# Optimization experiments

Hardware: AMD Instinct MI355X
Metric: run time of the kernel (lower is better)

## Reference

```python
import jax, jax.numpy as jnp
import numpy as np

NUM_HEADS = 8


def setup_inputs() -> dict:
    key = jax.random.key(0)
    ks = jax.random.split(key, 6)
    B, C, H, W = 64, 512, 16, 16
    x = jax.random.normal(ks[0], (B, C, H, W), dtype=jnp.float32)
    qkv_w = jax.random.normal(ks[1], (3 * C, C), dtype=jnp.float32) * (C ** -0.5)
    qkv_b = jax.random.normal(ks[2], (3 * C,), dtype=jnp.float32) * 0.02
    out_w = jax.random.normal(ks[3], (C, C), dtype=jnp.float32) * (C ** -0.5)
    out_b = jax.random.normal(ks[4], (C,), dtype=jnp.float32) * 0.02
    rel_pos_enc = jax.random.normal(ks[5], (NUM_HEADS, 2 * 16 - 1, 2 * 16 - 1), dtype=jnp.float32) * 0.02
    return {"x": x, "qkv_w": qkv_w, "qkv_b": qkv_b, "out_w": out_w,
            "out_b": out_b, "rel_pos_enc": rel_pos_enc}


def _attention(x, qkv_w, qkv_b, out_w, out_b, rel_pos_enc):
    B, C, H, W = x.shape
    heads = rel_pos_enc.shape[0]
    hd = C // heads
    N = H * W

    # 1x1 conv qkv projection == pointwise GEMM over channels
    qkv = jnp.einsum('bchw,oc->bohw', x, qkv_w) + qkv_b[None, :, None, None]
    q, k, v = jnp.split(qkv, 3, axis=1)  # each (B, C, H, W)
    q = q.reshape(B, heads, hd, N)
    k = k.reshape(B, heads, hd, N)
    v = v.reshape(B, heads, hd, N)

    attn = jnp.einsum('bhdn,bhdm->bhnm', q, k) * (hd ** -0.5)  # (B,h,N,N)

    # gathered 2D relative position bias: bias[head,(h1,w1),(h2,w2)] =
    #   rel_pos_enc[head, h1-h2+15, w1-w2+15]
    h_idx = (jnp.arange(H)[:, None] - jnp.arange(H)[None, :]) + 16 - 1  # (H,H)
    w_idx = (jnp.arange(W)[:, None] - jnp.arange(W)[None, :]) + 16 - 1  # (W,W)
    bias = rel_pos_enc[:, h_idx[:, None, :, None], w_idx[None, :, None, :]]  # (h,H,W,H,W)
    bias = bias.reshape(heads, N, N)

    attn = jax.nn.softmax(attn + bias[None], axis=-1)
    out = jnp.einsum('bhnm,bhdm->bhdn', attn, v).reshape(B, C, H, W)
    out = jnp.einsum('bchw,oc->bohw', out, out_w) + out_b[None, :, None, None]
    return out


def reference(x, qkv_w, qkv_b, out_w, out_b, rel_pos_enc):
    return _attention(x, qkv_w, qkv_b, out_w, out_b, rel_pos_enc)
```

## Files before the change

### kernel.cpp

```cpp
#include <hip/hip_runtime.h>

typedef __attribute__((ext_vector_type(8))) short short8;
typedef __attribute__((ext_vector_type(4))) float floatx4;
typedef __attribute__((ext_vector_type(4))) int   intx4;

#define MFMA16(a,b,c) __builtin_amdgcn_mfma_f32_16x16x32_bf16((a),(b),(c),0,0,0)

static __device__ __forceinline__ unsigned short f2bf(float f){
    unsigned int u = __float_as_uint(f);
    u = (u + 0x7FFFu + ((u >> 16) & 1u)) >> 16;
    return (unsigned short)u;
}

static __device__ __forceinline__ unsigned int pkbf(float lo, float hi){
    unsigned int r;
    asm("v_cvt_pk_bf16_f32 %0, %1, %2" : "=v"(r) : "v"(lo), "v"(hi));
    return r;
}

static __device__ __forceinline__ void async16(const unsigned short* g, const unsigned short* l){
    __builtin_amdgcn_global_load_lds(
        (const __attribute__((address_space(1))) unsigned int*)g,
        (__attribute__((address_space(3))) unsigned int*)l, 16, 0, 0);
}

__global__ __launch_bounds__(256) void k_prep(const float* __restrict__ x,
                                              unsigned short* __restrict__ xT,
                                              const float* __restrict__ qkvw,
                                              unsigned short* __restrict__ wqkv,
                                              const float* __restrict__ outw,
                                              unsigned short* __restrict__ wout,
                                              const float* __restrict__ rel,
                                              unsigned short* __restrict__ Bp){
    __shared__ unsigned short tile[64][78];
    const int bid = blockIdx.x;
    const int tid = threadIdx.x;
    if (bid < 2048){
        const int c0 = (bid & 7) * 64;
        const int n0 = ((bid >> 3) & 3) * 64;
        const int b  = bid >> 5;
        const int chunk = tid & 7;
        const int r     = tid >> 3;
        const float*    src = x  + (size_t)b * 131072;
        unsigned short* dst = xT + (size_t)b * 131072;
#pragma unroll
        for (int it = 0; it < 2; ++it){
            int c = r + it * 32;
            const float* p = src + (size_t)(c0 + c) * 256 + n0 + chunk * 8;
            float4 f0 = *(const float4*)(p);
            float4 f1 = *(const float4*)(p + 4);
            short8 v;
            v[0]=(short)f2bf(f0.x); v[1]=(short)f2bf(f0.y); v[2]=(short)f2bf(f0.z); v[3]=(short)f2bf(f0.w);
            v[4]=(short)f2bf(f1.x); v[5]=(short)f2bf(f1.y); v[6]=(short)f2bf(f1.z); v[7]=(short)f2bf(f1.w);
            *(short8*)&tile[c][chunk * 8] = v;
        }
        __syncthreads();
#pragma unroll
        for (int it = 0; it < 2; ++it){
            int n = r + it * 32;
            short8 o;
#pragma unroll
            for (int e = 0; e < 8; ++e) o[e] = (short)tile[chunk * 8 + e][n];
            *(short8*)(dst + (size_t)(n0 + n) * 512 + c0 + chunk * 8) = o;
        }
    } else if (bid < 3072){
        int i = (bid - 2048) * 256 + tid;
        const float* s; unsigned short* d; int j;
        if (i < 196608){ s = qkvw; d = wqkv; j = i; }
        else { j = i - 196608; if (j >= 65536) return; s = outw; d = wout; }
        float4 f = *(const float4*)(s + (size_t)j * 4);
        uint2 v;
        v.x = (unsigned int)f2bf(f.x) | ((unsigned int)f2bf(f.y) << 16);
        v.y = (unsigned int)f2bf(f.z) | ((unsigned int)f2bf(f.w) << 16);
        *(uint2*)(d + (size_t)j * 4) = v;
    } else {
        int idx  = (bid - 3072) * 256 + tid;
        int lane = idx & 63;
        int ct   = (idx >> 6) & 15;
        int pp   = (idx >> 10) & 1;
        int wv   = (idx >> 11) & 7;
        int h    = idx >> 14;
        int token = wv * 32 + pp * 16 + (lane & 15);
        int key0  = 32 * (ct >> 1) + 8 * (lane >> 4) + 4 * (ct & 1);
        int th = token >> 4, tw = token & 15;
        int kh = key0 >> 4,  kw0 = key0 & 15;
        int base = h * 961 + (th - kh + 15) * 31 + (tw - kw0 + 15);
        float v0 = rel[base]     * 1.44269504f;
        float v1 = rel[base - 1] * 1.44269504f;
        float v2 = rel[base - 2] * 1.44269504f;
        float v3 = rel[base - 3] * 1.44269504f;
        uint2 o; o.x = pkbf(v0, v1); o.y = pkbf(v2, v3);
        *(uint2*)(Bp + (size_t)idx * 4) = o;
    }
}

__global__ __launch_bounds__(512, 2) void k_fused(const unsigned short* __restrict__ xT,
                                                  const unsigned short* __restrict__ wbf,
                                                  const float* __restrict__ qkvb,
                                                  const unsigned short* __restrict__ Bp,
                                                  unsigned short* __restrict__ ao){
    __shared__ unsigned short SH[77824];
    const int XS = 0;
    const int WS = 16384;
    const int QS = 28672;
    const int KS = 45056;
    const int VS = 61440;

    const int bid  = blockIdx.x;
    const int xcd  = bid & 7;
    const int slot = bid >> 3;
    const int b = xcd * 8 + (slot & 7);
    const int h = slot >> 3;
    const int tid  = threadIdx.x;
    const int wave = tid >> 6;
    const int lane = tid & 63;
    const int lrow = lane & 15;
    const int lgrp = lane >> 4;
    const int mq = wave >> 1;
    const int nh = wave & 1;

    floatx4 acc[4][6];
#pragma unroll
    for (int i = 0; i < 4; ++i)
#pragma unroll
        for (int j = 0; j < 6; ++j){ floatx4 z = {0.f,0.f,0.f,0.f}; acc[i][j] = z; }

    const unsigned short* xb = xT + (size_t)(b * 256) * 512;
    const unsigned short* xsrc[4]; int xdo[4];
#pragma unroll
    for (int c = 0; c < 4; ++c){
        int s   = (c * 8 + wave) * 64 + lane;
        int row = s >> 3, pch = s & 7;
        int sch = pch ^ (row & 7);
        xsrc[c] = xb + (size_t)row * 512 + sch * 8;
        xdo[c]  = (c * 8 + wave) * 512;
    }
    const unsigned short* wsrc[3]; int wdo[3];
#pragma unroll
    for (int c = 0; c < 3; ++c){
        int s   = (c * 8 + wave) * 64 + lane;
        int row = s >> 3, pch = s & 7;
        int sch = pch ^ (row & 7);
        int grow = (row >> 6) * 512 + h * 64 + (row & 63);
        wsrc[c] = wbf + (size_t)grow * 512 + sch * 8;
        wdo[c]  = (c * 8 + wave) * 512;
    }

    auto stageA = [&](int XBs, int WBs, int kk){
#pragma unroll
        for (int c = 0; c < 4; ++c) async16(xsrc[c] + kk, &SH[XBs + xdo[c]]);
#pragma unroll
        for (int c = 0; c < 3; ++c) async16(wsrc[c] + kk, &SH[WBs + wdo[c]]);
    };
    auto compA = [&](int XBs, int WBs){
#pragma unroll
        for (int ks = 0; ks < 2; ++ks){
            short8 af[4], bq[6];
#pragma unroll
            for (int mt = 0; mt < 4; ++mt){
                int row = mq * 64 + mt * 16 + lrow;
                int pch = (ks * 4 + lgrp) ^ (row & 7);
                af[mt] = *(const short8*)&SH[XBs + row * 64 + pch * 8];
            }
#pragma unroll
            for (int nt = 0; nt < 6; ++nt){
                int row = nh * 96 + nt * 16 + lrow;
                int pch = (ks * 4 + lgrp) ^ (row & 7);
                bq[nt] = *(const short8*)&SH[WBs + row * 64 + pch * 8];
            }
#pragma unroll
            for (int mt = 0; mt < 4; ++mt)
#pragma unroll
                for (int nt = 0; nt < 6; ++nt)
                    acc[mt][nt] = MFMA16(af[mt], bq[nt], acc[mt][nt]);
        }
    };

    stageA(XS, WS, 0);
    stageA(QS, KS, 64);
#pragma unroll
    for (int t2 = 0; t2 < 4; ++t2){
        asm volatile("s_waitcnt vmcnt(7)" ::: "memory");
        __builtin_amdgcn_s_barrier();
        asm volatile("" ::: "memory");
        compA(XS, WS);
        asm volatile("" ::: "memory");
        if (t2 < 3){
            __builtin_amdgcn_s_barrier();
            stageA(XS, WS, t2 * 128 + 128);
            asm volatile("s_waitcnt vmcnt(7)" ::: "memory");
        } else {
            asm volatile("s_waitcnt vmcnt(0)" ::: "memory");
        }
        __builtin_amdgcn_s_barrier();
        asm volatile("" ::: "memory");
        compA(QS, KS);
        asm volatile("" ::: "memory");
        __builtin_amdgcn_s_barrier();
        if (t2 < 3) stageA(QS, KS, t2 * 128 + 192);
    }

    const uint2* bpw = (const uint2*)Bp + (((size_t)h * 8 + wave) * 2) * 1024 + lane;
    uint2 bA[16], bB[16];
#pragma unroll
    for (int ct = 0; ct < 16; ++ct){
        bA[ct] = bpw[ct * 64];
        bB[ct] = bpw[(16 + ct) * 64];
    }
    asm volatile("" ::: "memory");

#pragma unroll
    for (int mt = 0; mt < 4; ++mt){
#pragma unroll
        for (int nt = 0; nt < 6; ++nt){
            int col = nh * 96 + nt * 16 + lrow;
            int seg = col >> 6, off = col & 63;
            float bv = qkvb[seg * 512 + h * 64 + off];
            int token0 = mq * 64 + mt * 16 + lgrp * 4;
            if (seg == 2){
                int lch = token0 >> 3;
                int pch = (lch & 24) | ((lch & 7) ^ (off & 7));
                uint2 vv;
                vv.x = pkbf(acc[mt][nt][0] + bv, acc[mt][nt][1] + bv);
                vv.y = pkbf(acc[mt][nt][2] + bv, acc[mt][nt][3] + bv);
                *(uint2*)&SH[VS + off * 256 + pch * 8 + (lgrp & 1) * 4] = vv;
            } else if (seg == 1){
#pragma unroll
                for (int r = 0; r < 4; ++r){
                    int token = token0 + r;
                    int kslot = (token & ~0x1C) | ((token & 4) << 2) | ((token & 0x18) >> 1);
                    int pch   = (off >> 3) ^ (kslot & 7);
                    SH[KS + kslot * 64 + pch * 8 + (off & 7)] = f2bf(acc[mt][nt][r] + bv);
                }
            } else {
#pragma unroll
                for (int r = 0; r < 4; ++r){
                    int token = token0 + r;
                    int pch   = (off >> 3) ^ (token & 7);
                    SH[QS + token * 64 + pch * 8 + (off & 7)] =
                        f2bf((acc[mt][nt][r] + bv) * 0.18033688f);
                }
            }
        }
    }
    __syncthreads();

    short8 aq[2][2];
#pragma unroll
    for (int pp = 0; pp < 2; ++pp)
#pragma unroll
        for (int kc = 0; kc < 2; ++kc){
            int row = wave * 32 + pp * 16 + lrow;
            int pch = (kc * 4 + lgrp) ^ (row & 7);
            aq[pp][kc] = *(const short8*)&SH[QS + row * 64 + pch * 8];
        }

    floatx4 st0[16], st1[16];
    __builtin_amdgcn_s_setprio(1);
#pragma unroll
    for (int ct = 0; ct < 16; ++ct){
        int row  = ct * 16 + lrow;
        int pch0 = lgrp ^ (row & 7);
        short8 k0 = *(const short8*)&SH[KS + row * 64 + pch0 * 8];
        short8 k1 = *(const short8*)&SH[KS + row * 64 + (pch0 ^ 4) * 8];
        floatx4 z0, z1;
        z0[0] = __uint_as_float(bA[ct].x << 16);
        z0[1] = __uint_as_float(bA[ct].x & 0xFFFF0000u);
        z0[2] = __uint_as_float(bA[ct].y << 16);
        z0[3] = __uint_as_float(bA[ct].y & 0xFFFF0000u);
        z1[0] = __uint_as_float(bB[ct].x << 16);
        z1[1] = __uint_as_float(bB[ct].x & 0xFFFF0000u);
        z1[2] = __uint_as_float(bB[ct].y << 16);
        z1[3] = __uint_as_float(bB[ct].y & 0xFFFF0000u);
        z0 = MFMA16(k0, aq[0][0], z0);
        z0 = MFMA16(k1, aq[0][1], z0);
        z1 = MFMA16(k0, aq[1][0], z1);
        z1 = MFMA16(k1, aq[1][1], z1);
        st0[ct] = z0; st1[ct] = z1;
    }
    __builtin_amdgcn_s_setprio(0);

    float inv0, inv1;
    {
        float p0=0.f,p1=0.f,p2=0.f,p3=0.f;
#pragma unroll
        for (int ct = 0; ct < 16; ++ct){
            float e0 = __builtin_amdgcn_exp2f(st0[ct][0]); st0[ct][0]=e0; p0+=e0;
            float e1 = __builtin_amdgcn_exp2f(st0[ct][1]); st0[ct][1]=e1; p1+=e1;
            float e2 = __builtin_amdgcn_exp2f(st0[ct][2]); st0[ct][2]=e2; p2+=e2;
            float e3 = __builtin_amdgcn_exp2f(st0[ct][3]); st0[ct][3]=e3; p3+=e3;
        }
        float s = (p0+p1)+(p2+p3);
        s += __shfl_xor(s, 16, 64);
        s += __shfl_xor(s, 32, 64);
        inv0 = 1.f / s;
    }
    {
        float p0=0.f,p1=0.f,p2=0.f,p3=0.f;
#pragma unroll
        for (int ct = 0; ct < 16; ++ct){
            float e0 = __builtin_amdgcn_exp2f(st1[ct][0]); st1[ct][0]=e0; p0+=e0;
            float e1 = __builtin_amdgcn_exp2f(st1[ct][1]); st1[ct][1]=e1; p1+=e1;
            float e2 = __builtin_amdgcn_exp2f(st1[ct][2]); st1[ct][2]=e2; p2+=e2;
            float e3 = __builtin_amdgcn_exp2f(st1[ct][3]); st1[ct][3]=e3; p3+=e3;
        }
        float s = (p0+p1)+(p2+p3);
        s += __shfl_xor(s, 16, 64);
        s += __shfl_xor(s, 32, 64);
        inv1 = 1.f / s;
    }

    intx4 pf0[8], pf1[8];
#pragma unroll
    for (int ms = 0; ms < 8; ++ms){
        intx4 t0_, t1_;
        t0_.x = (int)pkbf(st0[2*ms  ][0], st0[2*ms  ][1]);
        t0_.y = (int)pkbf(st0[2*ms  ][2], st0[2*ms  ][3]);
        t0_.z = (int)pkbf(st0[2*ms+1][0], st0[2*ms+1][1]);
        t0_.w = (int)pkbf(st0[2*ms+1][2], st0[2*ms+1][3]);
        pf0[ms] = t0_;
        t1_.x = (int)pkbf(st1[2*ms  ][0], st1[2*ms  ][1]);
        t1_.y = (int)pkbf(st1[2*ms  ][2], st1[2*ms  ][3]);
        t1_.z = (int)pkbf(st1[2*ms+1][0], st1[2*ms+1][1]);
        t1_.w = (int)pkbf(st1[2*ms+1][2], st1[2*ms+1][3]);
        pf1[ms] = t1_;
    }

    unsigned short* aob = ao + (size_t)(b * 256) * 512 + h * 64;
    const int n0 = wave * 32 + lrow;
    __builtin_amdgcn_s_setprio(1);
#pragma unroll
    for (int dt = 0; dt < 4; ++dt){
        floatx4 a0 = {0.f,0.f,0.f,0.f}, a1 = {0.f,0.f,0.f,0.f};
#pragma unroll
        for (int ms = 0; ms < 8; ++ms){
            int row = dt * 16 + lrow;
            int lch = ms * 4 + lgrp;
            int pch = (lch & 24) | ((lch & 7) ^ (row & 7));
            short8 vb = *(const short8*)&SH[VS + row * 256 + pch * 8];
            a0 = MFMA16(vb, __builtin_bit_cast(short8, pf0[ms]), a0);
            a1 = MFMA16(vb, __builtin_bit_cast(short8, pf1[ms]), a1);
        }
        uint2 o0, o1;
        o0.x = pkbf(a0[0] * inv0, a0[1] * inv0);
        o0.y = pkbf(a0[2] * inv0, a0[3] * inv0);
        *(uint2*)(aob + (size_t)n0 * 512 + dt * 16 + lgrp * 4) = o0;
        o1.x = pkbf(a1[0] * inv1, a1[1] * inv1);
        o1.y = pkbf(a1[2] * inv1, a1[3] * inv1);
        *(uint2*)(aob + (size_t)(n0 + 16) * 512 + dt * 16 + lgrp * 4) = o1;
    }
    __builtin_amdgcn_s_setprio(0);
}

__global__ __launch_bounds__(256, 2) void k_out(const unsigned short* __restrict__ ao,
                                                const unsigned short* __restrict__ wbf,
                                                const float* __restrict__ bias,
                                                float* __restrict__ out){
    __shared__ unsigned short Ash[2][2][128][32];
    __shared__ unsigned short Bsh[2][2][128][32];
    const int bid  = blockIdx.x;
    const int xcd  = bid & 7;
    const int slot = bid >> 3;
    const int t0 = (xcd * 16 + (slot & 15)) * 128;
    const int o0 = (slot >> 4) * 128;
    const int tid  = threadIdx.x;
    const int wave = tid >> 6;
    const int lane = tid & 63;
    const int lrow = lane & 15;
    const int wm   = (wave >> 1) * 64;
    const int wn   = (wave & 1) * 64;
    const int ld_row = wave * 32 + (lane >> 2);
    const int ld_col = (((lane & 3) ^ ((lane >> 3) & 3))) * 8;
    const int pcho = (((lane >> 4) ^ ((lrow >> 1) & 3))) * 8;

    floatx4 acc[4][4];
#pragma unroll
    for (int i = 0; i < 4; ++i)
#pragma unroll
        for (int j = 0; j < 4; ++j){ floatx4 z = {0.f,0.f,0.f,0.f}; acc[i][j] = z; }

    const unsigned short* gA = wbf + (size_t)(o0 + ld_row) * 512 + ld_col;
    const unsigned short* gB = ao  + (size_t)(t0 + ld_row) * 512 + ld_col;

    auto stage = [&](int d, int kk){
        async16(gA + kk,                 &Ash[d][0][wave * 32][0]);
        async16(gA + kk + 16 * 512,      &Ash[d][0][wave * 32 + 16][0]);
        async16(gA + kk + 32,            &Ash[d][1][wave * 32][0]);
        async16(gA + kk + 32 + 16 * 512, &Ash[d][1][wave * 32 + 16][0]);
        async16(gB + kk,                 &Bsh[d][0][wave * 32][0]);
        async16(gB + kk + 16 * 512,      &Bsh[d][0][wave * 32 + 16][0]);
        async16(gB + kk + 32,            &Bsh[d][1][wave * 32][0]);
        async16(gB + kk + 32 + 16 * 512, &Bsh[d][1][wave * 32 + 16][0]);
    };
    auto comp = [&](int d){
#pragma unroll
        for (int s = 0; s < 2; ++s){
            short8 af[4], bq[4];
#pragma unroll
            for (int mt = 0; mt < 4; ++mt) af[mt] = *(const short8*)&Ash[d][s][wm + mt*16 + lrow][pcho];
#pragma unroll
            for (int nt = 0; nt < 4; ++nt) bq[nt] = *(const short8*)&Bsh[d][s][wn + nt*16 + lrow][pcho];
#pragma unroll
            for (int mt = 0; mt < 4; ++mt)
#pragma unroll
                for (int nt = 0; nt < 4; ++nt)
                    acc[mt][nt] = MFMA16(af[mt], bq[nt], acc[mt][nt]);
        }
    };

    stage(0, 0);
    stage(1, 64);
#pragma unroll
    for (int t2 = 0; t2 < 4; ++t2){
        asm volatile("s_waitcnt vmcnt(8)" ::: "memory");
        __builtin_amdgcn_s_barrier();
        asm volatile("" ::: "memory");
        comp(0);
        asm volatile("" ::: "memory");
        if (t2 < 3){
            __builtin_amdgcn_s_barrier();
            stage(0, t2 * 128 + 128);
            asm volatile("s_waitcnt vmcnt(8)" ::: "memory");
        } else {
            asm volatile("s_waitcnt vmcnt(0)" ::: "memory");
        }
        __builtin_amdgcn_s_barrier();
        asm volatile("" ::: "memory");
        comp(1);
        asm volatile("" ::: "memory");
        __builtin_amdgcn_s_barrier();
        if (t2 < 3) stage(1, t2 * 128 + 192);
    }
#pragma unroll
    for (int mt = 0; mt < 4; ++mt){
        int orow0 = o0 + wm + mt*16 + (lane >> 4) * 4;
#pragma unroll
        for (int nt = 0; nt < 4; ++nt){
            int tcol = t0 + wn + nt*16 + lrow;
            int bb = tcol >> 8, nn = tcol & 255;
#pragma unroll
            for (int r = 0; r < 4; ++r){
                float bv = bias[orow0 + r];
                out[(size_t)(bb * 512 + orow0 + r) * 256 + nn] = acc[mt][nt][r] + bv;
            }
        }
    }
}

extern "C" void kernel_launch(void* const* d_in, const int* in_sizes, int n_in,
                              void* d_out, int out_size, void* d_ws, size_t ws_size,
                              hipStream_t stream){
    const float* x    = (const float*)d_in[0];
    const float* qkvw = (const float*)d_in[1];
    const float* qkvb = (const float*)d_in[2];
    const float* outw = (const float*)d_in[3];
    const float* outb = (const float*)d_in[4];
    const float* rel  = (const float*)d_in[5];
    float* out = (float*)d_out;

    const size_t XT_OFF = 0;
    const size_t AO_OFF = 16777216;
    const size_t W_OFF  = 33554432;
    const size_t NEED   = W_OFF + 4194304;
    if (ws_size < NEED) return;

    char* ws = (char*)d_ws;
    unsigned short* xT = (unsigned short*)(ws + XT_OFF);
    unsigned short* ao = (unsigned short*)(ws + AO_OFF);
    unsigned short* wqkv_bf = (unsigned short*)(ws + W_OFF);
    unsigned short* wout_bf = (unsigned short*)(ws + W_OFF + 2097152);
    unsigned short* Bp      = (unsigned short*)(ws + W_OFF + 2621440);

    hipLaunchKernelGGL(k_prep,  dim3(3584), dim3(256), 0, stream,
                       x, xT, qkvw, wqkv_bf, outw, wout_bf, rel, Bp);
    hipLaunchKernelGGL(k_fused, dim3(512),  dim3(512), 0, stream,
                       xT, wqkv_bf, qkvb, Bp, ao);
    hipLaunchKernelGGL(k_out,   dim3(512),  dim3(256), 0, stream,
                       ao, wout_bf, outb, out);
}
```

Before: 149.0 us.

## Process two heads per fused block and prefetch second head's operands during attention

Each fused block now handles two heads (h0 and h0+4) for one batch element, halving the grid from 512 to 256 blocks. The first k-slices of x and the second head's weights are issued asynchronously while the first head's attention runs, hiding part of the second projection's load latency. The cost is that x is reloaded per head rather than shared, and with half as many blocks on 256 CUs the GPU gets less block-level parallelism and lower occupancy.

```diff
diff --git a/kernel.cpp b/kernel.cpp
--- a/kernel.cpp
+++ b/kernel.cpp
@@ -109,8 +109,8 @@
     const int bid  = blockIdx.x;
     const int xcd  = bid & 7;
     const int slot = bid >> 3;
-    const int b = xcd * 8 + (slot & 7);
-    const int h = slot >> 3;
+    const int b  = xcd * 8 + (slot & 7);
+    const int h0 = slot >> 3;
     const int tid  = threadIdx.x;
     const int wave = tid >> 6;
     const int lane = tid & 63;
@@ -119,12 +119,6 @@
     const int mq = wave >> 1;
     const int nh = wave & 1;
 
-    floatx4 acc[4][6];
-#pragma unroll
-    for (int i = 0; i < 4; ++i)
-#pragma unroll
-        for (int j = 0; j < 6; ++j){ floatx4 z = {0.f,0.f,0.f,0.f}; acc[i][j] = z; }
-
     const unsigned short* xb = xT + (size_t)(b * 256) * 512;
     const unsigned short* xsrc[4]; int xdo[4];
 #pragma unroll
@@ -135,24 +129,28 @@
         xsrc[c] = xb + (size_t)row * 512 + sch * 8;
         xdo[c]  = (c * 8 + wave) * 512;
     }
-    const unsigned short* wsrc[3]; int wdo[3];
-#pragma unroll
-    for (int c = 0; c < 3; ++c){
-        int s   = (c * 8 + wave) * 64 + lane;
-        int row = s >> 3, pch = s & 7;
-        int sch = pch ^ (row & 7);
-        int grow = (row >> 6) * 512 + h * 64 + (row & 63);
-        wsrc[c] = wbf + (size_t)grow * 512 + sch * 8;
-        wdo[c]  = (c * 8 + wave) * 512;
-    }
-
-    auto stageA = [&](int XBs, int WBs, int kk){
+    const unsigned short* wsrcP[2][3]; int wdo[3];
+#pragma unroll
+    for (int pr = 0; pr < 2; ++pr)
+#pragma unroll
+        for (int c = 0; c < 3; ++c){
+            int s   = (c * 8 + wave) * 64 + lane;
+            int row = s >> 3, pch = s & 7;
+            int sch = pch ^ (row & 7);
+            int grow = (row >> 6) * 512 + (h0 + pr * 4) * 64 + (row & 63);
+            wsrcP[pr][c] = wbf + (size_t)grow * 512 + sch * 8;
+            wdo[c]  = (c * 8 + wave) * 512;
+        }
+
+    auto stageX = [&](int XBs, int kk){
 #pragma unroll
         for (int c = 0; c < 4; ++c) async16(xsrc[c] + kk, &SH[XBs + xdo[c]]);
-#pragma unroll
-        for (int c = 0; c < 3; ++c) async16(wsrc[c] + kk, &SH[WBs + wdo[c]]);
     };
-    auto compA = [&](int XBs, int WBs){
+    auto stageW = [&](int pr, int WBs, int kk){
+#pragma unroll
+        for (int c = 0; c < 3; ++c) async16(wsrcP[pr][c] + kk, &SH[WBs + wdo[c]]);
+    };
+    auto compA = [&](floatx4 (&acc)[4][6], int XBs, int WBs){
 #pragma unroll
         for (int ks = 0; ks < 2; ++ks){
             short8 af[4], bq[6];
@@ -176,180 +174,202 @@
         }
     };
 
-    stageA(XS, WS, 0);
-    stageA(QS, KS, 64);
-#pragma unroll
-    for (int t2 = 0; t2 < 4; ++t2){
-        asm volatile("s_waitcnt vmcnt(7)" ::: "memory");
-        __builtin_amdgcn_s_barrier();
+#pragma unroll
+    for (int pr = 0; pr < 2; ++pr){
+        const int h = h0 + pr * 4;
+
+        floatx4 acc[4][6];
+#pragma unroll
+        for (int i = 0; i < 4; ++i)
+#pragma unroll
+            for (int j = 0; j < 6; ++j){ floatx4 z = {0.f,0.f,0.f,0.f}; acc[i][j] = z; }
+
+        if (pr == 0){
+            stageX(XS, 0);  stageW(0, WS, 0);
+            stageX(QS, 64); stageW(0, KS, 64);
+        } else {
+            __builtin_amdgcn_s_barrier();
+            asm volatile("" ::: "memory");
+            stageX(QS, 64); stageW(1, KS, 64);
+        }
+
+#pragma unroll
+        for (int t2 = 0; t2 < 4; ++t2){
+            asm volatile("s_waitcnt vmcnt(7)" ::: "memory");
+            __builtin_amdgcn_s_barrier();
+            asm volatile("" ::: "memory");
+            compA(acc, XS, WS);
+            asm volatile("" ::: "memory");
+            if (t2 < 3){
+                __builtin_amdgcn_s_barrier();
+                stageX(XS, t2 * 128 + 128); stageW(pr, WS, t2 * 128 + 128);
+                asm volatile("s_waitcnt vmcnt(7)" ::: "memory");
+            } else {
+                asm volatile("s_waitcnt vmcnt(0)" ::: "memory");
+            }
+            __builtin_amdgcn_s_barrier();
+            asm volatile("" ::: "memory");
+            compA(acc, QS, KS);
+            asm volatile("" ::: "memory");
+            __builtin_amdgcn_s_barrier();
+            if (t2 < 3){ stageX(QS, t2 * 128 + 192); stageW(pr, KS, t2 * 128 + 192); }
+        }
+
+        const uint2* bpw = (const uint2*)Bp + (((size_t)h * 8 + wave) * 2) * 1024 + lane;
+        uint2 bA[16], bB[16];
+#pragma unroll
+        for (int ct = 0; ct < 16; ++ct){
+            bA[ct] = bpw[ct * 64];
+            bB[ct] = bpw[(16 + ct) * 64];
+        }
         asm volatile("" ::: "memory");
-        compA(XS, WS);
-        asm volatile("" ::: "memory");
-        if (t2 < 3){
-            __builtin_amdgcn_s_barrier();
-            stageA(XS, WS, t2 * 128 + 128);
-            asm volatile("s_waitcnt vmcnt(7)" ::: "memory");
-        } else {
-            asm volatile("s_waitcnt vmcnt(0)" ::: "memory");
-        }
-        __builtin_amdgcn_s_barrier();
-        asm volatile("" ::: "memory");
-        compA(QS, KS);
-        asm volatile("" ::: "memory");
-        __builtin_amdgcn_s_barrier();
-        if (t2 < 3) stageA(QS, KS, t2 * 128 + 192);
+
+#pragma unroll
+        for (int mt = 0; mt < 4; ++mt){
+#pragma unroll
+            for (int nt = 0; nt < 6; ++nt){
+                int col = nh * 96 + nt * 16 + lrow;
+                int seg = col >> 6, off = col & 63;
+                float bv = qkvb[seg * 512 + h * 64 + off];
+                int token0 = mq * 64 + mt * 16 + lgrp * 4;
+                if (seg == 2){
+                    int lch = token0 >> 3;
+                    int pch = (lch & 24) | ((lch & 7) ^ (off & 7));
+                    uint2 vv;
+                    vv.x = pkbf(acc[mt][nt][0] + bv, acc[mt][nt][1] + bv);
+                    vv.y = pkbf(acc[mt][nt][2] + bv, acc[mt][nt][3] + bv);
+                    *(uint2*)&SH[VS + off * 256 + pch * 8 + (lgrp & 1) * 4] = vv;
+                } else if (seg == 1){
+#pragma unroll
+                    for (int r = 0; r < 4; ++r){
+                        int token = token0 + r;
+                        int kslot = (token & ~0x1C) | ((token & 4) << 2) | ((token & 0x18) >> 1);
+                        int pch   = (off >> 3) ^ (kslot & 7);
+                        SH[KS + kslot * 64 + pch * 8 + (off & 7)] = f2bf(acc[mt][nt][r] + bv);
+                    }
+                } else {
+#pragma unroll
+                    for (int r = 0; r < 4; ++r){
+                        int token = token0 + r;
+                        int pch   = (off >> 3) ^ (token & 7);
+                        SH[QS + token * 64 + pch * 8 + (off & 7)] =
+                            f2bf((acc[mt][nt][r] + bv) * 0.18033688f);
+                    }
+                }
+            }
+        }
+        __syncthreads();
+
+        short8 aq[2][2];
+#pragma unroll
+        for (int pp = 0; pp < 2; ++pp)
+#pragma unroll
+            for (int kc = 0; kc < 2; ++kc){
+                int row = wave * 32 + pp * 16 + lrow;
+                int pch = (kc * 4 + lgrp) ^ (row & 7);
+                aq[pp][kc] = *(const short8*)&SH[QS + row * 64 + pch * 8];
+            }
+
+        if (pr == 0){
+            stageX(XS, 0); stageW(1, WS, 0);
+        }
+
+        floatx4 st0[16], st1[16];
+        __builtin_amdgcn_s_setprio(1);
+#pragma unroll
+        for (int ct = 0; ct < 16; ++ct){
+            int row  = ct * 16 + lrow;
+            int pch0 = lgrp ^ (row & 7);
+            short8 k0 = *(const short8*)&SH[KS + row * 64 + pch0 * 8];
+            short8 k1 = *(const short8*)&SH[KS + row * 64 + (pch0 ^ 4) * 8];
+            floatx4 z0, z1;
+            z0[0] = __uint_as_float(bA[ct].x << 16);
+            z0[1] = __uint_as_float(bA[ct].x & 0xFFFF0000u);
+            z0[2] = __uint_as_float(bA[ct].y << 16);
+            z0[3] = __uint_as_float(bA[ct].y & 0xFFFF0000u);
+            z1[0] = __uint_as_float(bB[ct].x << 16);
+            z1[1] = __uint_as_float(bB[ct].x & 0xFFFF0000u);
+            z1[2] = __uint_as_float(bB[ct].y << 16);
+            z1[3] = __uint_as_float(bB[ct].y & 0xFFFF0000u);
+            z0 = MFMA16(k0, aq[0][0], z0);
+            z0 = MFMA16(k1, aq[0][1], z0);
+            z1 = MFMA16(k0, aq[1][0], z1);
+            z1 = MFMA16(k1, aq[1][1], z1);
+            st0[ct] = z0; st1[ct] = z1;
+        }
+        __builtin_amdgcn_s_setprio(0);
+
+        float inv0, inv1;
+        {
+            float p0=0.f,p1=0.f,p2=0.f,p3=0.f;
+#pragma unroll
+            for (int ct = 0; ct < 16; ++ct){
+                float e0 = __builtin_amdgcn_exp2f(st0[ct][0]); st0[ct][0]=e0; p0+=e0;
+                float e1 = __builtin_amdgcn_exp2f(st0[ct][1]); st0[ct][1]=e1; p1+=e1;
+                float e2 = __builtin_amdgcn_exp2f(st0[ct][2]); st0[ct][2]=e2; p2+=e2;
+                float e3 = __builtin_amdgcn_exp2f(st0[ct][3]); st0[ct][3]=e3; p3+=e3;
+            }
+            float s = (p0+p1)+(p2+p3);
+            s += __shfl_xor(s, 16, 64);
+            s += __shfl_xor(s, 32, 64);
+            inv0 = 1.f / s;
+        }
+        {
+            float p0=0.f,p1=0.f,p2=0.f,p3=0.f;
+#pragma unroll
+            for (int ct = 0; ct < 16; ++ct){
+                float e0 = __builtin_amdgcn_exp2f(st1[ct][0]); st1[ct][0]=e0; p0+=e0;
+                float e1 = __builtin_amdgcn_exp2f(st1[ct][1]); st1[ct][1]=e1; p1+=e1;
+                float e2 = __builtin_amdgcn_exp2f(st1[ct][2]); st1[ct][2]=e2; p2+=e2;
+                float e3 = __builtin_amdgcn_exp2f(st1[ct][3]); st1[ct][3]=e3; p3+=e3;
+            }
+            float s = (p0+p1)+(p2+p3);
+            s += __shfl_xor(s, 16, 64);
+            s += __shfl_xor(s, 32, 64);
+            inv1 = 1.f / s;
+        }
+
+        intx4 pf0[8], pf1[8];
+#pragma unroll
+        for (int ms = 0; ms < 8; ++ms){
+            intx4 t0_, t1_;
+            t0_.x = (int)pkbf(st0[2*ms  ][0], st0[2*ms  ][1]);
+            t0_.y = (int)pkbf(st0[2*ms  ][2], st0[2*ms  ][3]);
+            t0_.z = (int)pkbf(st0[2*ms+1][0], st0[2*ms+1][1]);
+            t0_.w = (int)pkbf(st0[2*ms+1][2], st0[2*ms+1][3]);
+            pf0[ms] = t0_;
+            t1_.x = (int)pkbf(st1[2*ms  ][0], st1[2*ms  ][1]);
+            t1_.y = (int)pkbf(st1[2*ms  ][2], st1[2*ms  ][3]);
+            t1_.z = (int)pkbf(st1[2*ms+1][0], st1[2*ms+1][1]);
+            t1_.w = (int)pkbf(st1[2*ms+1][2], st1[2*ms+1][3]);
+            pf1[ms] = t1_;
+        }
+
+        unsigned short* aob = ao + (size_t)(b * 256) * 512 + h * 64;
+        const int n0 = wave * 32 + lrow;
+        __builtin_amdgcn_s_setprio(1);
+#pragma unroll
+        for (int dt = 0; dt < 4; ++dt){
+            floatx4 a0 = {0.f,0.f,0.f,0.f}, a1 = {0.f,0.f,0.f,0.f};
+#pragma unroll
+            for (int ms = 0; ms < 8; ++ms){
+                int row = dt * 16 + lrow;
+                int lch = ms * 4 + lgrp;
+                int pch = (lch & 24) | ((lch & 7) ^ (row & 7));
+                short8 vb = *(const short8*)&SH[VS + row * 256 + pch * 8];
+                a0 = MFMA16(vb, __builtin_bit_cast(short8, pf0[ms]), a0);
+                a1 = MFMA16(vb, __builtin_bit_cast(short8, pf1[ms]), a1);
+            }
+            uint2 o0, o1;
+            o0.x = pkbf(a0[0] * inv0, a0[1] * inv0);
+            o0.y = pkbf(a0[2] * inv0, a0[3] * inv0);
+            *(uint2*)(aob + (size_t)n0 * 512 + dt * 16 + lgrp * 4) = o0;
+            o1.x = pkbf(a1[0] * inv1, a1[1] * inv1);
+            o1.y = pkbf(a1[2] * inv1, a1[3] * inv1);
+            *(uint2*)(aob + (size_t)(n0 + 16) * 512 + dt * 16 + lgrp * 4) = o1;
+        }
+        __builtin_amdgcn_s_setprio(0);
     }
-
-    const uint2* bpw = (const uint2*)Bp + (((size_t)h * 8 + wave) * 2) * 1024 + lane;
-    uint2 bA[16], bB[16];
-#pragma unroll
-    for (int ct = 0; ct < 16; ++ct){
-        bA[ct] = bpw[ct * 64];
-        bB[ct] = bpw[(16 + ct) * 64];
-    }
-    asm volatile("" ::: "memory");
-
-#pragma unroll
-    for (int mt = 0; mt < 4; ++mt){
-#pragma unroll
-        for (int nt = 0; nt < 6; ++nt){
-            int col = nh * 96 + nt * 16 + lrow;
-            int seg = col >> 6, off = col & 63;
-            float bv = qkvb[seg * 512 + h * 64 + off];
-            int token0 = mq * 64 + mt * 16 + lgrp * 4;
-            if (seg == 2){
-                int lch = token0 >> 3;
-                int pch = (lch & 24) | ((lch & 7) ^ (off & 7));
-                uint2 vv;
-                vv.x = pkbf(acc[mt][nt][0] + bv, acc[mt][nt][1] + bv);
-                vv.y = pkbf(acc[mt][nt][2] + bv, acc[mt][nt][3] + bv);
-                *(uint2*)&SH[VS + off * 256 + pch * 8 + (lgrp & 1) * 4] = vv;
-            } else if (seg == 1){
-#pragma unroll
-                for (int r = 0; r < 4; ++r){
-                    int token = token0 + r;
-                    int kslot = (token & ~0x1C) | ((token & 4) << 2) | ((token & 0x18) >> 1);
-                    int pch   = (off >> 3) ^ (kslot & 7);
-                    SH[KS + kslot * 64 + pch * 8 + (off & 7)] = f2bf(acc[mt][nt][r] + bv);
-                }
-            } else {
-#pragma unroll
-                for (int r = 0; r < 4; ++r){
-                    int token = token0 + r;
-                    int pch   = (off >> 3) ^ (token & 7);
-                    SH[QS + token * 64 + pch * 8 + (off & 7)] =
-                        f2bf((acc[mt][nt][r] + bv) * 0.18033688f);
-                }
-            }
-        }
-    }
-    __syncthreads();
-
-    short8 aq[2][2];
-#pragma unroll
-    for (int pp = 0; pp < 2; ++pp)
-#pragma unroll
-        for (int kc = 0; kc < 2; ++kc){
-            int row = wave * 32 + pp * 16 + lrow;
-            int pch = (kc * 4 + lgrp) ^ (row & 7);
-            aq[pp][kc] = *(const short8*)&SH[QS + row * 64 + pch * 8];
-        }
-
-    floatx4 st0[16], st1[16];
-    __builtin_amdgcn_s_setprio(1);
-#pragma unroll
-    for (int ct = 0; ct < 16; ++ct){
-        int row  = ct * 16 + lrow;
-        int pch0 = lgrp ^ (row & 7);
-        short8 k0 = *(const short8*)&SH[KS + row * 64 + pch0 * 8];
-        short8 k1 = *(const short8*)&SH[KS + row * 64 + (pch0 ^ 4) * 8];
-        floatx4 z0, z1;
-        z0[0] = __uint_as_float(bA[ct].x << 16);
-        z0[1] = __uint_as_float(bA[ct].x & 0xFFFF0000u);
-        z0[2] = __uint_as_float(bA[ct].y << 16);
-        z0[3] = __uint_as_float(bA[ct].y & 0xFFFF0000u);
-        z1[0] = __uint_as_float(bB[ct].x << 16);
-        z1[1] = __uint_as_float(bB[ct].x & 0xFFFF0000u);
-        z1[2] = __uint_as_float(bB[ct].y << 16);
-        z1[3] = __uint_as_float(bB[ct].y & 0xFFFF0000u);
-        z0 = MFMA16(k0, aq[0][0], z0);
-        z0 = MFMA16(k1, aq[0][1], z0);
-        z1 = MFMA16(k0, aq[1][0], z1);
-        z1 = MFMA16(k1, aq[1][1], z1);
-        st0[ct] = z0; st1[ct] = z1;
-    }
-    __builtin_amdgcn_s_setprio(0);
-
-    float inv0, inv1;
-    {
-        float p0=0.f,p1=0.f,p2=0.f,p3=0.f;
-#pragma unroll
-        for (int ct = 0; ct < 16; ++ct){
-            float e0 = __builtin_amdgcn_exp2f(st0[ct][0]); st0[ct][0]=e0; p0+=e0;
-            float e1 = __builtin_amdgcn_exp2f(st0[ct][1]); st0[ct][1]=e1; p1+=e1;
-            float e2 = __builtin_amdgcn_exp2f(st0[ct][2]); st0[ct][2]=e2; p2+=e2;
-            float e3 = __builtin_amdgcn_exp2f(st0[ct][3]); st0[ct][3]=e3; p3+=e3;
-        }
-        float s = (p0+p1)+(p2+p3);
-        s += __shfl_xor(s, 16, 64);
-        s += __shfl_xor(s, 32, 64);
-        inv0 = 1.f / s;
-    }
-    {
-        float p0=0.f,p1=0.f,p2=0.f,p3=0.f;
-#pragma unroll
-        for (int ct = 0; ct < 16; ++ct){
-            float e0 = __builtin_amdgcn_exp2f(st1[ct][0]); st1[ct][0]=e0; p0+=e0;
-            float e1 = __builtin_amdgcn_exp2f(st1[ct][1]); st1[ct][1]=e1; p1+=e1;
-            float e2 = __builtin_amdgcn_exp2f(st1[ct][2]); st1[ct][2]=e2; p2+=e2;
-            float e3 = __builtin_amdgcn_exp2f(st1[ct][3]); st1[ct][3]=e3; p3+=e3;
-        }
-        float s = (p0+p1)+(p2+p3);
-        s += __shfl_xor(s, 16, 64);
-        s += __shfl_xor(s, 32, 64);
-        inv1 = 1.f / s;
-    }
-
-    intx4 pf0[8], pf1[8];
-#pragma unroll
-    for (int ms = 0; ms < 8; ++ms){
-        intx4 t0_, t1_;
-        t0_.x = (int)pkbf(st0[2*ms  ][0], st0[2*ms  ][1]);
-        t0_.y = (int)pkbf(st0[2*ms  ][2], st0[2*ms  ][3]);
-        t0_.z = (int)pkbf(st0[2*ms+1][0], st0[2*ms+1][1]);
-        t0_.w = (int)pkbf(st0[2*ms+1][2], st0[2*ms+1][3]);
-        pf0[ms] = t0_;
-        t1_.x = (int)pkbf(st1[2*ms  ][0], st1[2*ms  ][1]);
-        t1_.y = (int)pkbf(st1[2*ms  ][2], st1[2*ms  ][3]);
-        t1_.z = (int)pkbf(st1[2*ms+1][0], st1[2*ms+1][1]);
-        t1_.w = (int)pkbf(st1[2*ms+1][2], st1[2*ms+1][3]);
-        pf1[ms] = t1_;
-    }
-
-    unsigned short* aob = ao + (size_t)(b * 256) * 512 + h * 64;
-    const int n0 = wave * 32 + lrow;
-    __builtin_amdgcn_s_setprio(1);
-#pragma unroll
-    for (int dt = 0; dt < 4; ++dt){
-        floatx4 a0 = {0.f,0.f,0.f,0.f}, a1 = {0.f,0.f,0.f,0.f};
-#pragma unroll
-        for (int ms = 0; ms < 8; ++ms){
-            int row = dt * 16 + lrow;
-            int lch = ms * 4 + lgrp;
-            int pch = (lch & 24) | ((lch & 7) ^ (row & 7));
-            short8 vb = *(const short8*)&SH[VS + row * 256 + pch * 8];
-            a0 = MFMA16(vb, __builtin_bit_cast(short8, pf0[ms]), a0);
-            a1 = MFMA16(vb, __builtin_bit_cast(short8, pf1[ms]), a1);
-        }
-        uint2 o0, o1;
-        o0.x = pkbf(a0[0] * inv0, a0[1] * inv0);
-        o0.y = pkbf(a0[2] * inv0, a0[3] * inv0);
-        *(uint2*)(aob + (size_t)n0 * 512 + dt * 16 + lgrp * 4) = o0;
-        o1.x = pkbf(a1[0] * inv1, a1[1] * inv1);
-        o1.y = pkbf(a1[2] * inv1, a1[3] * inv1);
-        *(uint2*)(aob + (size_t)(n0 + 16) * 512 + dt * 16 + lgrp * 4) = o1;
-    }
-    __builtin_amdgcn_s_setprio(0);
 }
 
 __global__ __launch_bounds__(256, 2) void k_out(const unsigned short* __restrict__ ao,
@@ -473,7 +493,7 @@
 
     hipLaunchKernelGGL(k_prep,  dim3(3584), dim3(256), 0, stream,
                        x, xT, qkvw, wqkv_bf, outw, wout_bf, rel, Bp);
-    hipLaunchKernelGGL(k_fused, dim3(512),  dim3(512), 0, stream,
+    hipLaunchKernelGGL(k_fused, dim3(256),  dim3(512), 0, stream,
                        xT, wqkv_bf, qkvb, Bp, ao);
     hipLaunchKernelGGL(k_out,   dim3(512),  dim3(256), 0, stream,
                        ao, wout_bf, outb, out);
```

New measurement: 183.6 us. 23.2% more time.
